# Optimization experiments

Hardware: AMD Instinct MI355X
Metric: run time of the kernel (lower is better)

The kernel has to match this reference:

```python
import jax, jax.numpy as jnp
import numpy as np

EMBED_DIM = 1024
NUM_HEADS = 16
HEAD_DIM = EMBED_DIM // NUM_HEADS


def setup_inputs() -> dict:
    key = jax.random.key(0)
    ks = jax.random.split(key, 9)
    B, S, D = 2, 2048, EMBED_DIM
    scale = 1.0 / np.sqrt(D)
    x = jax.random.normal(ks[0], (B, S, D), dtype=jnp.float32)
    Wq = jax.random.normal(ks[1], (D, D), dtype=jnp.float32) * scale
    Wk = jax.random.normal(ks[2], (D, D), dtype=jnp.float32) * scale
    Wv = jax.random.normal(ks[3], (D, D), dtype=jnp.float32) * scale
    Wo = jax.random.normal(ks[4], (D, D), dtype=jnp.float32) * scale
    bq = jnp.zeros((D,), jnp.float32)
    bk = jnp.zeros((D,), jnp.float32)
    bv = jnp.zeros((D,), jnp.float32)
    bo = jnp.zeros((D,), jnp.float32)
    return {"x": x, "Wq": Wq, "bq": bq, "Wk": Wk, "bk": bk,
            "Wv": Wv, "bv": bv, "Wo": Wo, "bo": bo}


def reference(x, Wq, bq, Wk, bk, Wv, bv, Wo, bo):
    B, S, D = x.shape
    H, Dh = NUM_HEADS, HEAD_DIM
    # QKV projections -> [B, H, S, Dh]
    q = (x @ Wq + bq).reshape(B, S, H, Dh).transpose(0, 2, 1, 3)
    k = (x @ Wk + bk).reshape(B, S, H, Dh).transpose(0, 2, 1, 3)
    v = (x @ Wv + bv).reshape(B, S, H, Dh).transpose(0, 2, 1, 3)
    # scores [B, H, S, S], scaled by sqrt(head_dim)
    scores = jnp.einsum('bhqd,bhkd->bhqk', q, k) / jnp.sqrt(jnp.float32(Dh))
    attn = jax.nn.softmax(scores, axis=-1)
    out = jnp.einsum('bhqk,bhkd->bhqd', attn, v)  # [B, H, S, Dh]
    out = out.transpose(0, 2, 1, 3).reshape(B, S, D)
    return out @ Wo + bo
```

## Files before the change

### kernel.cpp

```cpp
#include <hip/hip_runtime.h>
#include <hip/hip_bf16.h>

typedef short bf16x8 __attribute__((ext_vector_type(8)));
typedef float f32x4 __attribute__((ext_vector_type(4)));

#define MFMA16(a, b, c) __builtin_amdgcn_mfma_f32_16x16x32_bf16((a), (b), (c), 0, 0, 0)

static constexpr int B_ = 2, S_ = 2048, D_ = 1024, H_ = 16, DH = 64;
static constexpr int M_ = B_ * S_;
static constexpr int K_ = D_;

static __device__ __forceinline__ ushort f2bf(float f) {
    __hip_bfloat16 h = __float2bfloat16(f);
    return *reinterpret_cast<ushort*>(&h);
}

static __device__ __forceinline__ void gload16(const ushort* g, ushort* l) {
    __builtin_amdgcn_global_load_lds((const __attribute__((address_space(1))) void*)g,
                                     (__attribute__((address_space(3))) void*)l, 16, 0, 0);
}

__global__ __launch_bounds__(256) void cvt_f2b(const float* __restrict__ in,
                                               ushort* __restrict__ out) {
    int i = blockIdx.x * blockDim.x + threadIdx.x;
    float4 v = reinterpret_cast<const float4*>(in)[i];
    ushort4 o;
    o.x = f2bf(v.x); o.y = f2bf(v.y); o.z = f2bf(v.z); o.w = f2bf(v.w);
    reinterpret_cast<ushort4*>(out)[i] = o;
}

__global__ __launch_bounds__(256) void transpose_w4(const float* __restrict__ W0,
                                                    const float* __restrict__ W1,
                                                    const float* __restrict__ W2,
                                                    const float* __restrict__ W3,
                                                    ushort* __restrict__ T0,
                                                    ushort* __restrict__ T1,
                                                    ushort* __restrict__ T2,
                                                    ushort* __restrict__ T3) {
    __shared__ float tile[32][33];
    int z = blockIdx.z;
    const float* W = (z == 0) ? W0 : (z == 1) ? W1 : (z == 2) ? W2 : W3;
    ushort* T = (z == 0) ? T0 : (z == 1) ? T1 : (z == 2) ? T2 : T3;
    int bx = blockIdx.x, by = blockIdx.y;
    int tx = threadIdx.x, ty = threadIdx.y;
#pragma unroll
    for (int i = 0; i < 4; i++)
        tile[ty + i * 8][tx] = W[(by * 32 + ty + i * 8) * D_ + bx * 32 + tx];
    __syncthreads();
#pragma unroll
    for (int i = 0; i < 4; i++)
        T[(bx * 32 + ty + i * 8) * K_ + by * 32 + tx] = f2bf(tile[tx][ty + i * 8]);
}

template <int MODE, int TM>
__global__ __launch_bounds__(256, 4) void gemmNT(const ushort* __restrict__ A,
                                                 const ushort* __restrict__ Wt,
                                                 const float* __restrict__ bias_q,
                                                 const float* __restrict__ bias_k,
                                                 const float* __restrict__ bias_v,
                                                 ushort* __restrict__ Qb,
                                                 ushort* __restrict__ Kb,
                                                 ushort* __restrict__ Vtb,
                                                 float* __restrict__ outf) {
    constexpr int MI = TM / 32;
    __shared__ __align__(16) ushort As[TM * 32];
    __shared__ __align__(16) ushort Bs[64 * 32];

    int m0 = blockIdx.x * TM;
    int n0 = blockIdx.y * 64;
    int t = threadIdx.x;
    int lane = t & 63, w = t >> 6;
    int ln = lane & 15, lq = lane >> 4;
    int wm = (w >> 1) * (TM / 2), wn = (w & 1) * 32;

    f32x4 acc[MI][2];
#pragma unroll
    for (int i = 0; i < MI; i++)
#pragma unroll
        for (int j = 0; j < 2; j++) acc[i][j] = f32x4{0.f, 0.f, 0.f, 0.f};

    for (int k0 = 0; k0 < K_; k0 += 32) {
#pragma unroll
        for (int c = t; c < TM * 4; c += 256)
            gload16(A + (size_t)(m0 + (c >> 2)) * K_ + k0 + (c & 3) * 8, As + c * 8);
        gload16(Wt + (size_t)(n0 + (t >> 2)) * K_ + k0 + (t & 3) * 8, Bs + t * 8);
        __syncthreads();
        bf16x8 af[MI], bfr[2];
#pragma unroll
        for (int i = 0; i < MI; i++)
            af[i] = *reinterpret_cast<const bf16x8*>(As + (wm + i * 16 + ln) * 32 + lq * 8);
#pragma unroll
        for (int j = 0; j < 2; j++)
            bfr[j] = *reinterpret_cast<const bf16x8*>(Bs + (wn + j * 16 + ln) * 32 + lq * 8);
#pragma unroll
        for (int i = 0; i < MI; i++)
#pragma unroll
            for (int j = 0; j < 2; j++)
                acc[i][j] = MFMA16(af[i], bfr[j], acc[i][j]);
        __syncthreads();
    }

#pragma unroll
    for (int j = 0; j < 2; j++) {
        int n = n0 + wn + j * 16 + ln;
        if (MODE == 1) {
            float bv = bias_q[n];
#pragma unroll
            for (int i = 0; i < MI; i++) {
#pragma unroll
                for (int r = 0; r < 4; r++) {
                    int m = m0 + wm + i * 16 + lq * 4 + r;
                    outf[(size_t)m * D_ + n] = acc[i][j][r] + bv;
                }
            }
        } else {
            int which = n >> 10, nn = n & 1023, h = nn >> 6, dh = nn & 63;
            const float* bp = (which == 0) ? bias_q : (which == 1) ? bias_k : bias_v;
            float bv = bp[nn];
            if (which == 2) {
#pragma unroll
                for (int i = 0; i < MI; i++) {
                    int m = m0 + wm + i * 16 + lq * 4;
                    int b = m >> 11, s0 = m & 2047;
                    ushort4 o4;
                    o4.x = f2bf(acc[i][j][0] + bv);
                    o4.y = f2bf(acc[i][j][1] + bv);
                    o4.z = f2bf(acc[i][j][2] + bv);
                    o4.w = f2bf(acc[i][j][3] + bv);
                    *reinterpret_cast<ushort4*>(Vtb + (((size_t)(b * H_ + h) * DH) + dh) * S_ + s0) = o4;
                }
            } else {
                ushort* dst = (which == 0) ? Qb : Kb;
#pragma unroll
                for (int i = 0; i < MI; i++) {
#pragma unroll
                    for (int r = 0; r < 4; r++) {
                        int m = m0 + wm + i * 16 + lq * 4 + r;
                        int b = m >> 11, s = m & 2047;
                        dst[(((b * H_ + h) * S_) + s) * DH + dh] = f2bf(acc[i][j][r] + bv);
                    }
                }
            }
        }
    }
}

__global__ __launch_bounds__(256, 4) void attn32d(const ushort* __restrict__ Q,
                                                  const ushort* __restrict__ K,
                                                  const ushort* __restrict__ Vt,
                                                  ushort* __restrict__ O) {
    __shared__ __align__(16) ushort Kl[2][2048];
    __shared__ __align__(16) ushort Vl[2][2048];
    __shared__ __align__(16) short Pl[4][16 * 36];

    int bid = blockIdx.x;
    int qb = bid & 31;
    int bh = bid >> 5;
    int t = threadIdx.x;
    int lane = t & 63, w = t >> 6;
    int ln = lane & 15, lq = lane >> 4;
    int qt = qb * 4 + w;

    const ushort* Qp = Q + (size_t)bh * S_ * DH;
    const ushort* Kp = K + (size_t)bh * S_ * DH;
    const ushort* Vp = Vt + (size_t)bh * DH * S_;

    bf16x8 qf0 = *reinterpret_cast<const bf16x8*>(Qp + (qt * 16 + ln) * DH + lq * 8);
    bf16x8 qf1 = *reinterpret_cast<const bf16x8*>(Qp + (qt * 16 + ln) * DH + 32 + lq * 8);

    const ushort* Kg = Kp + (size_t)(t & 31) * DH + (t >> 5) * 8;
    const ushort* Vg = Vp + (size_t)(t >> 2) * S_ + (t & 3) * 8;

    f32x4 o_acc[4];
    float l_part[4] = {0.f, 0.f, 0.f, 0.f};
#pragma unroll
    for (int nt = 0; nt < 4; nt++) o_acc[nt] = f32x4{0.f, 0.f, 0.f, 0.f};

    gload16(Kg, Kl[0] + t * 8);
    gload16(Vg, Vl[0] + t * 8);

    const float kSc = 0.18033688011112042f;

    for (int kt = 0; kt < S_ / 32; kt++) {
        __syncthreads();
        int cur = kt & 1;
        if (kt + 1 < S_ / 32) {
            int kb = (kt + 1) * 32;
            gload16(Kg + (size_t)kb * DH, Kl[cur ^ 1] + t * 8);
            gload16(Vg + kb, Vl[cur ^ 1] + t * 8);
        }
        const ushort* Kc = Kl[cur];
        const ushort* Vc = Vl[cur];

        f32x4 sc[2];
#pragma unroll
        for (int nt = 0; nt < 2; nt++) {
            bf16x8 kf0 = *reinterpret_cast<const bf16x8*>(Kc + (lq * 32 + nt * 16 + ln) * 8);
            bf16x8 kf1 = *reinterpret_cast<const bf16x8*>(Kc + ((4 + lq) * 32 + nt * 16 + ln) * 8);
            f32x4 c = {0.f, 0.f, 0.f, 0.f};
            c = MFMA16(qf0, kf0, c);
            c = MFMA16(qf1, kf1, c);
            sc[nt] = c;
        }
#pragma unroll
        for (int nt = 0; nt < 2; nt++)
#pragma unroll
            for (int r = 0; r < 4; r++) {
                float p = exp2f(sc[nt][r] * kSc);
                l_part[r] += p;
                Pl[w][(lq * 4 + r) * 36 + nt * 16 + ln] = (short)f2bf(p);
            }
        bf16x8 pf = *reinterpret_cast<const bf16x8*>(&Pl[w][ln * 36 + lq * 8]);
#pragma unroll
        for (int nt = 0; nt < 4; nt++) {
            bf16x8 vf = *reinterpret_cast<const bf16x8*>(Vc + ((nt * 16 + ln) * 4 + lq) * 8);
            o_acc[nt] = MFMA16(pf, vf, o_acc[nt]);
        }
    }

    float linv[4];
#pragma unroll
    for (int r = 0; r < 4; r++) {
        float l = l_part[r];
#pragma unroll
        for (int d = 1; d < 16; d <<= 1) l += __shfl_xor(l, d, 64);
        linv[r] = 1.0f / l;
    }
    int b = bh >> 4, h = bh & 15;
#pragma unroll
    for (int nt = 0; nt < 4; nt++)
#pragma unroll
        for (int r = 0; r < 4; r++) {
            int s = qt * 16 + lq * 4 + r;
            O[((b * S_ + s) * H_ + h) * DH + nt * 16 + ln] =
                f2bf(o_acc[nt][r] * linv[r]);
        }
}

extern "C" void kernel_launch(void* const* d_in, const int* in_sizes, int n_in,
                              void* d_out, int out_size, void* d_ws, size_t ws_size,
                              hipStream_t stream) {
    const float* x  = (const float*)d_in[0];
    const float* Wq = (const float*)d_in[1];
    const float* bq = (const float*)d_in[2];
    const float* Wk = (const float*)d_in[3];
    const float* bk = (const float*)d_in[4];
    const float* Wv = (const float*)d_in[5];
    const float* bv = (const float*)d_in[6];
    const float* Wo = (const float*)d_in[7];
    const float* bo = (const float*)d_in[8];
    float* out = (float*)d_out;

    char* ws = (char*)d_ws;
    const size_t MB = 1024 * 1024;
    ushort* wtq = (ushort*)(ws + 0 * MB);
    ushort* wtk = (ushort*)(ws + 2 * MB);
    ushort* wtv = (ushort*)(ws + 4 * MB);
    ushort* wto = (ushort*)(ws + 6 * MB);
    ushort* xb  = (ushort*)(ws + 8 * MB);
    ushort* Qb  = (ushort*)(ws + 16 * MB);
    ushort* Kb  = (ushort*)(ws + 24 * MB);
    ushort* Vtb = (ushort*)(ws + 32 * MB);
    ushort* AO  = (ushort*)(ws + 40 * MB);

    cvt_f2b<<<(M_ * K_ / 4) / 256, 256, 0, stream>>>(x, xb);

    transpose_w4<<<dim3(32, 32, 4), dim3(32, 8), 0, stream>>>(
        Wq, Wk, Wv, Wo, wtq, wtk, wtv, wto);

    gemmNT<0, 128><<<dim3(M_ / 128, 3072 / 64), 256, 0, stream>>>(
        xb, wtq, bq, bk, bv, Qb, Kb, Vtb, nullptr);

    attn32d<<<32 * 32, 256, 0, stream>>>(Qb, Kb, Vtb, AO);

    gemmNT<1, 64><<<dim3(M_ / 64, D_ / 64), 256, 0, stream>>>(
        AO, wto, bo, nullptr, nullptr, nullptr, nullptr, nullptr, out);
}
```

Measured before the change: 224.7 us.

## Enlarge GEMM tiles to 128x128/128x64 and remap V tile LDS layout

Replaces the GEMM kernel with a 128-row tile variant. QKV uses 128x128 tiles and the output projection 128x64 tiles, with global pointers precomputed outside the k-loop and occupancy hint lowered to 3. The goal is more reuse per LDS load and fewer blocks. The attention kernel's V tile load and read mapping is also changed to a lane-contiguous layout, aiming to reduce LDS bank conflicts on the V fragment reads. Larger tiles raise register pressure and, for the output GEMM, halve the block count, which may underfill the GPU.

```diff
diff --git a/kernel.cpp b/kernel.cpp
--- a/kernel.cpp
+++ b/kernel.cpp
@@ -52,61 +52,71 @@
         T[(bx * 32 + ty + i * 8) * K_ + by * 32 + tx] = f2bf(tile[tx][ty + i * 8]);
 }
 
-template <int MODE, int TM>
-__global__ __launch_bounds__(256, 4) void gemmNT(const ushort* __restrict__ A,
-                                                 const ushort* __restrict__ Wt,
-                                                 const float* __restrict__ bias_q,
-                                                 const float* __restrict__ bias_k,
-                                                 const float* __restrict__ bias_v,
-                                                 ushort* __restrict__ Qb,
-                                                 ushort* __restrict__ Kb,
-                                                 ushort* __restrict__ Vtb,
-                                                 float* __restrict__ outf) {
-    constexpr int MI = TM / 32;
-    __shared__ __align__(16) ushort As[TM * 32];
-    __shared__ __align__(16) ushort Bs[64 * 32];
-
-    int m0 = blockIdx.x * TM;
-    int n0 = blockIdx.y * 64;
+template <int MODE, int TN>
+__global__ __launch_bounds__(256, 3) void gemm128(const ushort* __restrict__ A,
+                                                  const ushort* __restrict__ Wt,
+                                                  const float* __restrict__ bias_q,
+                                                  const float* __restrict__ bias_k,
+                                                  const float* __restrict__ bias_v,
+                                                  ushort* __restrict__ Qb,
+                                                  ushort* __restrict__ Kb,
+                                                  ushort* __restrict__ Vtb,
+                                                  float* __restrict__ outf) {
+    constexpr int NJ = TN / 32;
+    __shared__ __align__(16) ushort As[128 * 32];
+    __shared__ __align__(16) ushort Bs[TN * 32];
+
+    int m0 = blockIdx.x * 128;
+    int n0 = blockIdx.y * TN;
     int t = threadIdx.x;
     int lane = t & 63, w = t >> 6;
     int ln = lane & 15, lq = lane >> 4;
-    int wm = (w >> 1) * (TM / 2), wn = (w & 1) * 32;
-
-    f32x4 acc[MI][2];
-#pragma unroll
-    for (int i = 0; i < MI; i++)
-#pragma unroll
-        for (int j = 0; j < 2; j++) acc[i][j] = f32x4{0.f, 0.f, 0.f, 0.f};
+    int wm = (w >> 1) * 64, wn = (w & 1) * (TN / 2);
+
+    int c0 = t, c1 = t + 256;
+    const ushort* Ag0 = A + (size_t)(m0 + (c0 >> 2)) * K_ + (c0 & 3) * 8;
+    const ushort* Ag1 = A + (size_t)(m0 + (c1 >> 2)) * K_ + (c1 & 3) * 8;
+    const ushort* Bg0 = Wt + (size_t)(n0 + (c0 >> 2)) * K_ + (c0 & 3) * 8;
+    const ushort* Bg1 = Wt + (size_t)(n0 + (c1 >> 2)) * K_ + (c1 & 3) * 8;
+    ushort* Al0 = As + c0 * 8;
+    ushort* Al1 = As + c1 * 8;
+    ushort* Bl0 = Bs + c0 * 8;
+    ushort* Bl1 = Bs + c1 * 8;
+
+    f32x4 acc[4][NJ];
+#pragma unroll
+    for (int i = 0; i < 4; i++)
+#pragma unroll
+        for (int j = 0; j < NJ; j++) acc[i][j] = f32x4{0.f, 0.f, 0.f, 0.f};
 
     for (int k0 = 0; k0 < K_; k0 += 32) {
-#pragma unroll
-        for (int c = t; c < TM * 4; c += 256)
-            gload16(A + (size_t)(m0 + (c >> 2)) * K_ + k0 + (c & 3) * 8, As + c * 8);
-        gload16(Wt + (size_t)(n0 + (t >> 2)) * K_ + k0 + (t & 3) * 8, Bs + t * 8);
+        gload16(Ag0 + k0, Al0);
+        gload16(Ag1 + k0, Al1);
+        gload16(Bg0 + k0, Bl0);
+        if (TN == 128) gload16(Bg1 + k0, Bl1);
         __syncthreads();
-        bf16x8 af[MI], bfr[2];
-#pragma unroll
-        for (int i = 0; i < MI; i++)
+        bf16x8 af[4], bfr[NJ];
+#pragma unroll
+        for (int i = 0; i < 4; i++)
             af[i] = *reinterpret_cast<const bf16x8*>(As + (wm + i * 16 + ln) * 32 + lq * 8);
 #pragma unroll
-        for (int j = 0; j < 2; j++)
+        for (int j = 0; j < NJ; j++)
             bfr[j] = *reinterpret_cast<const bf16x8*>(Bs + (wn + j * 16 + ln) * 32 + lq * 8);
 #pragma unroll
-        for (int i = 0; i < MI; i++)
-#pragma unroll
-            for (int j = 0; j < 2; j++)
+        for (int i = 0; i < 4; i++)
+#pragma unroll
+            for (int j = 0; j < NJ; j++)
                 acc[i][j] = MFMA16(af[i], bfr[j], acc[i][j]);
         __syncthreads();
     }
 
 #pragma unroll
-    for (int j = 0; j < 2; j++) {
+    for (int j = 0; j < NJ; j++) {
         int n = n0 + wn + j * 16 + ln;
         if (MODE == 1) {
             float bv = bias_q[n];
 #pragma unroll
-            for (int i = 0; i < MI; i++) {
+            for (int i = 0; i < 4; i++) {
 #pragma unroll
                 for (int r = 0; r < 4; r++) {
                     int m = m0 + wm + i * 16 + lq * 4 + r;
@@ -119,7 +129,7 @@
             float bv = bp[nn];
             if (which == 2) {
 #pragma unroll
-                for (int i = 0; i < MI; i++) {
+                for (int i = 0; i < 4; i++) {
                     int m = m0 + wm + i * 16 + lq * 4;
                     int b = m >> 11, s0 = m & 2047;
                     ushort4 o4;
@@ -132,7 +142,7 @@
             } else {
                 ushort* dst = (which == 0) ? Qb : Kb;
 #pragma unroll
-                for (int i = 0; i < MI; i++) {
+                for (int i = 0; i < 4; i++) {
 #pragma unroll
                     for (int r = 0; r < 4; r++) {
                         int m = m0 + wm + i * 16 + lq * 4 + r;
@@ -169,7 +179,7 @@
     bf16x8 qf1 = *reinterpret_cast<const bf16x8*>(Qp + (qt * 16 + ln) * DH + 32 + lq * 8);
 
     const ushort* Kg = Kp + (size_t)(t & 31) * DH + (t >> 5) * 8;
-    const ushort* Vg = Vp + (size_t)(t >> 2) * S_ + (t & 3) * 8;
+    const ushort* Vg = Vp + (size_t)(t & 63) * S_ + (t >> 6) * 8;
 
     f32x4 o_acc[4];
     float l_part[4] = {0.f, 0.f, 0.f, 0.f};
@@ -213,7 +223,7 @@
         bf16x8 pf = *reinterpret_cast<const bf16x8*>(&Pl[w][ln * 36 + lq * 8]);
 #pragma unroll
         for (int nt = 0; nt < 4; nt++) {
-            bf16x8 vf = *reinterpret_cast<const bf16x8*>(Vc + ((nt * 16 + ln) * 4 + lq) * 8);
+            bf16x8 vf = *reinterpret_cast<const bf16x8*>(Vc + (lq * 64 + nt * 16 + ln) * 8);
             o_acc[nt] = MFMA16(pf, vf, o_acc[nt]);
         }
     }
@@ -268,11 +278,11 @@
     transpose_w4<<<dim3(32, 32, 4), dim3(32, 8), 0, stream>>>(
         Wq, Wk, Wv, Wo, wtq, wtk, wtv, wto);
 
-    gemmNT<0, 128><<<dim3(M_ / 128, 3072 / 64), 256, 0, stream>>>(
+    gemm128<0, 128><<<dim3(M_ / 128, 3072 / 128), 256, 0, stream>>>(
         xb, wtq, bq, bk, bv, Qb, Kb, Vtb, nullptr);
 
     attn32d<<<32 * 32, 256, 0, stream>>>(Qb, Kb, Vtb, AO);
 
-    gemmNT<1, 64><<<dim3(M_ / 64, D_ / 64), 256, 0, stream>>>(
+    gemm128<1, 64><<<dim3(M_ / 128, D_ / 64), 256, 0, stream>>>(
         AO, wto, bo, nullptr, nullptr, nullptr, nullptr, nullptr, out);
 }
```

Result: faster. 214.6 us (-4.5%).
